# Optimization experiments

Measured on AMD Instinct MI355X. Metric: run time of the kernel, lower is better.

Reference implementation:

```python
import jax, jax.numpy as jnp
import numpy as np

MODEL_DIM = 1024
NUM_HEADS = 16
HEAD_DIM = MODEL_DIM // NUM_HEADS
ROPE_BASE = 10000.0


def apply_rope_full(x):
    # RoPE applied over the FULL model_dim (before head split), interleaved pairs.
    B, S, D = x.shape
    half = D // 2
    inv_freq = 1.0 / (ROPE_BASE ** (jnp.arange(half, dtype=x.dtype) / half))  # [half]
    ang = jnp.arange(S, dtype=x.dtype)[:, None] * inv_freq[None, :]           # [S, half]
    cos, sin = jnp.cos(ang), jnp.sin(ang)
    x1 = x[..., 0::2]  # [B,S,half]
    x2 = x[..., 1::2]
    r1 = x1 * cos - x2 * sin
    r2 = x1 * sin + x2 * cos
    # re-interleave
    return jnp.stack([r1, r2], axis=-1).reshape(B, S, D)


def setup_inputs() -> dict:
    key = jax.random.key(0)
    ks = jax.random.split(key, 9)
    B, S, D = 4, 2048, MODEL_DIM
    sc = 1.0 / np.sqrt(D)
    inp = {
        "X": jax.random.normal(ks[0], (B, S, D), dtype=jnp.float32),
        "Wq": jax.random.normal(ks[1], (D, D), dtype=jnp.float32) * sc,
        "bq": jnp.zeros((D,), dtype=jnp.float32),
        "Wk": jax.random.normal(ks[2], (D, D), dtype=jnp.float32) * sc,
        "bk": jnp.zeros((D,), dtype=jnp.float32),
        "Wv": jax.random.normal(ks[3], (D, D), dtype=jnp.float32) * sc,
        "bv": jnp.zeros((D,), dtype=jnp.float32),
        "Wo": jax.random.normal(ks[4], (D, D), dtype=jnp.float32) * sc,
        "bo": jnp.zeros((D,), dtype=jnp.float32),
    }
    return inp


def reference(X, Wq, bq, Wk, bk, Wv, bv, Wo, bo):
    B, S, D = X.shape
    H, hd = NUM_HEADS, HEAD_DIM
    q = apply_rope_full(X @ Wq + bq)  # [B,S,D], RoPE on full dim as in source
    k = apply_rope_full(X @ Wk + bk)
    v = X @ Wv + bv
    # split heads (contiguous slices d1:d2 == reshape to [B,S,H,hd])
    qh = q.reshape(B, S, H, hd)
    kh = k.reshape(B, S, H, hd)
    vh = v.reshape(B, S, H, hd)
    scale = 1.0 / jnp.sqrt(jnp.asarray(hd, dtype=X.dtype))
    scores = jnp.einsum("bqhd,bkhd->bhqk", qh, kh) * scale  # [B,H,S,S]
    causal = jnp.tril(jnp.ones((S, S), dtype=bool))
    scores = jnp.where(causal[None, None], scores, -jnp.inf)
    weights = jax.nn.softmax(scores, axis=-1)
    attn = jnp.einsum("bhqk,bkhd->bqhd", weights, vh).reshape(B, S, D)
    return attn @ Wo + bo
```

## Files before the change

kernel.cpp:

```cpp
#include <hip/hip_runtime.h>

typedef unsigned short u16;
typedef unsigned int   u32;
typedef __attribute__((ext_vector_type(4))) float f32x4;
typedef __attribute__((ext_vector_type(8))) short short8;

#define MODEL_DIM 1024
#define SEQ 2048
#define BATCH 4
#define NHEAD 16
#define HDIM 64
#define MTOT (BATCH*SEQ)
#define ELEMS ((size_t)MTOT*MODEL_DIM)

__device__ __forceinline__ u16 f2bf(float f) {
    u32 u = __float_as_uint(f);
    u = (u + 0x7fffu + ((u >> 16) & 1u)) >> 16;
    return (u16)u;
}
__device__ __forceinline__ u32 pack2(float a, float b) {
    return (u32)f2bf(a) | ((u32)f2bf(b) << 16);
}
__device__ __forceinline__ u32 cvtpk(float lo, float hi) {
    u32 r;
    asm("v_cvt_pk_bf16_f32 %0, %1, %2" : "=v"(r) : "v"(lo), "v"(hi));
    return r;
}
__device__ __forceinline__ float exp2a(float x) {
    float r;
    asm("v_exp_f32 %0, %1" : "=v"(r) : "v"(x));
    return r;
}

#define GLOAD16(g, l) __builtin_amdgcn_global_load_lds(                        \
        (const __attribute__((address_space(1))) unsigned int*)(g),            \
        (__attribute__((address_space(3))) unsigned int*)(l), 16, 0, 0)

__global__ __launch_bounds__(256) void prep_k(const float* __restrict__ X,
                                              u16* __restrict__ Xb,
                                              const float* __restrict__ Wq,
                                              const float* __restrict__ Wk,
                                              const float* __restrict__ Wv,
                                              const float* __restrict__ Wo,
                                              u16* __restrict__ Wt) {
    const int bid = blockIdx.x, t = threadIdx.x;
    if (bid < 8192) {
        size_t i = ((size_t)bid * 256 + t) * 4;
        float4 v = *(const float4*)(X + i);
        uint2 o; o.x = pack2(v.x, v.y); o.y = pack2(v.z, v.w);
        *(uint2*)(Xb + i) = o;
        return;
    }
    __shared__ float tile[32][33];
    const int bid2 = bid - 8192;
    const int z = bid2 >> 10, rem = bid2 & 1023;
    const int by = rem >> 5, bx = rem & 31;
    const float* W = (z == 0) ? Wq : (z == 1) ? Wk : (z == 2) ? Wv : Wo;
    const int k0 = by * 32, n0 = bx * 32;
    const int x = t & 31, y = t >> 5;
    for (int i = 0; i < 4; ++i)
        tile[y + i * 8][x] = W[(size_t)(k0 + y + i * 8) * MODEL_DIM + n0 + x];
    __syncthreads();
    u16* out = Wt + ((size_t)z << 20);
    for (int i = 0; i < 4; ++i)
        out[(size_t)(n0 + y + i * 8) * MODEL_DIM + k0 + x] = f2bf(tile[x][y + i * 8]);
}

__global__ __launch_bounds__(512) void gemm256qkv_k(
        const u16* __restrict__ A, const u16* __restrict__ Wt,
        u16* __restrict__ Qb, u16* __restrict__ Kb, u32* __restrict__ VT,
        const float* __restrict__ bq, const float* __restrict__ bk,
        const float* __restrict__ bv) {
    __shared__ __align__(16) u16 Ls[49152];
    const int tid  = threadIdx.x;
    const int wv   = tid >> 6, lane = tid & 63;
    const int l15  = lane & 15, quad = lane >> 4;
    const int wr = wv >> 2, wc = wv & 3;
    const int m0 = blockIdx.x * 256;
    const int region = blockIdx.y >> 3;
    const int n0 = (blockIdx.y & 7) * 128;

    const u16* Ag = A + (size_t)m0 * MODEL_DIM;
    const u16* Bg = Wt + ((size_t)region << 20) + (size_t)n0 * MODEL_DIM;

    f32x4 acc[8][2] = {};

#define STAGE_A(kt, d, q) do {                                                 \
    const int kk0_ = (kt) * 64;                                                \
    int L_ = ((q) * 256 + wc * 64 + lane) * 16;                                \
    int P_ = L_ ^ (((L_ >> 7) & 7) << 4);                                      \
    GLOAD16(Ag + (size_t)(wr * 128 + (P_ >> 7)) * MODEL_DIM + kk0_             \
               + ((P_ & 127) >> 1),                                            \
            &Ls[(d) * 24576 + wr * 8192 + (L_ >> 1)]);                         \
} while (0)
#define STAGE_B(kt, d, q) do {                                                 \
    const int kk0_ = (kt) * 64;                                                \
    int L_ = ((q) * 512 + tid) * 16;                                           \
    int P_ = L_ ^ (((L_ >> 7) & 7) << 4);                                      \
    GLOAD16(Bg + (size_t)(P_ >> 7) * MODEL_DIM + kk0_ + ((P_ & 127) >> 1),     \
            &Ls[(d) * 24576 + 16384 + (L_ >> 1)]);                             \
} while (0)

#define LDA8Q(mf, ks) ({                                                       \
    int P_ = ((mf) * 16 + l15) * 128 + ((ks) * 4 + quad) * 16;                 \
    int L_ = P_ ^ (((P_ >> 7) & 7) << 4);                                      \
    *(const short8*)(ab + (L_ >> 1)); })
#define LDB8Q(nf, ks) ({                                                       \
    int P_ = (wc * 32 + (nf) * 16 + l15) * 128 + ((ks) * 4 + quad) * 16;       \
    int L_ = P_ ^ (((P_ >> 7) & 7) << 4);                                      \
    *(const short8*)(bbQ + (L_ >> 1)); })

#define PHASE_MFMA_Q(MH)                                                       \
    __builtin_amdgcn_s_setprio(1);                                             \
    _Pragma("unroll")                                                          \
    for (int j2 = 0; j2 < 4; ++j2)                                             \
        _Pragma("unroll")                                                      \
        for (int nf2 = 0; nf2 < 2; ++nf2)                                      \
            acc[(MH) * 4 + j2][nf2] = __builtin_amdgcn_mfma_f32_16x16x32_bf16( \
                af[j2], bf[nf2], acc[(MH) * 4 + j2][nf2], 0, 0, 0);            \
    __builtin_amdgcn_s_setprio(0);

    STAGE_A(0, 0, 0); STAGE_B(0, 0, 0);
    STAGE_A(0, 0, 1); STAGE_B(0, 0, 1);
    STAGE_A(0, 0, 2); STAGE_A(0, 0, 3);

    for (int t = 0; t < 16; ++t) {
        const int pp2 = t & 1;
        const u16* ab  = &Ls[pp2 * 24576 + wr * 8192];
        const u16* bbQ = &Ls[pp2 * 24576 + 16384];
        const int dn = pp2 ^ 1;
        const bool more = (t + 1) < 16;
        short8 af[4], bf[2];
        if (more) { STAGE_A(t + 1, dn, 0); STAGE_B(t + 1, dn, 0); }
        if (more) asm volatile("s_waitcnt vmcnt(2)" ::: "memory");
        else      asm volatile("s_waitcnt vmcnt(0)" ::: "memory");
        __builtin_amdgcn_s_barrier();
        __builtin_amdgcn_sched_barrier(0);
        #pragma unroll
        for (int nf = 0; nf < 2; ++nf) bf[nf] = LDB8Q(nf, 0);
        #pragma unroll
        for (int j = 0; j < 4; ++j) af[j] = LDA8Q(j, 0);
        PHASE_MFMA_Q(0)
        __builtin_amdgcn_s_barrier();
        #pragma unroll
        for (int j = 0; j < 4; ++j) af[j] = LDA8Q(4 + j, 0);
        if (more) { STAGE_A(t + 1, dn, 1); STAGE_B(t + 1, dn, 1); }
        __builtin_amdgcn_s_barrier();
        __builtin_amdgcn_sched_barrier(0);
        PHASE_MFMA_Q(1)
        __builtin_amdgcn_s_barrier();
        #pragma unroll
        for (int nf = 0; nf < 2; ++nf) bf[nf] = LDB8Q(nf, 1);
        #pragma unroll
        for (int j = 0; j < 4; ++j) af[j] = LDA8Q(j, 1);
        if (more) STAGE_A(t + 1, dn, 2);
        __builtin_amdgcn_s_barrier();
        __builtin_amdgcn_sched_barrier(0);
        PHASE_MFMA_Q(0)
        __builtin_amdgcn_s_barrier();
        #pragma unroll
        for (int j = 0; j < 4; ++j) af[j] = LDA8Q(4 + j, 1);
        if (more) STAGE_A(t + 1, dn, 3);
        __builtin_amdgcn_s_barrier();
        __builtin_amdgcn_sched_barrier(0);
        PHASE_MFMA_Q(1)
        __builtin_amdgcn_s_barrier();
    }

    if (region < 2) {
        const float* bias = region ? bk : bq;
        u16* dst = region ? Kb : Qb;
        const float qsc = region ? 1.0f : 0.125f * 1.44269504f;
        const float cfr = -0.017989922f;
        float invf[2];
        #pragma unroll
        for (int nf = 0; nf < 2; ++nf) {
            int c = n0 + wc * 32 + nf * 16 + l15;
            invf[nf] = __expf((float)(c >> 1) * cfr);
        }
        const float sgn = (l15 & 1) ? 1.0f : -1.0f;
        #pragma unroll
        for (int mf = 0; mf < 8; ++mf)
            #pragma unroll
            for (int r = 0; r < 4; ++r) {
                size_t rowg = (size_t)(m0 + wr * 128 + mf * 16 + quad * 4 + r);
                float fs = (float)(int)(rowg & 2047);
                #pragma unroll
                for (int nf = 0; nf < 2; ++nf) {
                    int c = n0 + wc * 32 + nf * 16 + l15;
                    float v = acc[mf][nf][r] + bias[c];
                    float mate = __shfl_xor(v, 1, 64);
                    float sn, cs;
                    __sincosf(fs * invf[nf], &sn, &cs);
                    float o = (v * cs + sgn * mate * sn) * qsc;
                    dst[rowg * MODEL_DIM + c] = f2bf(o);
                }
            }
    } else {
        const int b_ = m0 >> 11;
        const int s0 = m0 & 2047;
        #pragma unroll
        for (int nf = 0; nf < 2; ++nf) {
            int c = n0 + wc * 32 + nf * 16 + l15;
            float bvc = bv[c];
            u32* vtrow = VT + (size_t)((b_ * NHEAD + (c >> 6)) * HDIM
                                       + (c & 63)) * (SEQ / 2);
            #pragma unroll
            for (int mf = 0; mf < 8; ++mf) {
                int sb2 = s0 + wr * 128 + mf * 16 + quad * 4;
                uint2 w;
                w.x = cvtpk(acc[mf][nf][0] + bvc, acc[mf][nf][1] + bvc);
                w.y = cvtpk(acc[mf][nf][2] + bvc, acc[mf][nf][3] + bvc);
                *(uint2*)(vtrow + (sb2 >> 1)) = w;
            }
        }
    }
#undef STAGE_A
#undef STAGE_B
#undef LDA8Q
#undef LDB8Q
#undef PHASE_MFMA_Q
}

__global__ __launch_bounds__(512) void gemm256o_k(
        const u16* __restrict__ A, const u16* __restrict__ Wt,
        float* __restrict__ outO, const float* __restrict__ bo) {
    __shared__ __align__(16) u16 Ls[49152];
    const int tid  = threadIdx.x;
    const int wv   = tid >> 6, lane = tid & 63;
    const int l15  = lane & 15, quad = lane >> 4;
    const int wr = wv >> 2, wc = wv & 3;
    const int m0 = blockIdx.x * 256;
    const int n0 = blockIdx.y * 128;

    const u16* Ag = A + (size_t)m0 * MODEL_DIM;
    const u16* Bg = Wt + ((size_t)3 << 20) + (size_t)n0 * MODEL_DIM;

    f32x4 acc[8][2] = {};

#define STAGE_A(kt, d, q) do {                                                 \
    const int kk0_ = (kt) * 64;                                                \
    int L_ = ((q) * 256 + wc * 64 + lane) * 16;                                \
    int P_ = L_ ^ (((L_ >> 7) & 7) << 4);                                      \
    GLOAD16(Ag + (size_t)(wr * 128 + (P_ >> 7)) * MODEL_DIM + kk0_             \
               + ((P_ & 127) >> 1),                                            \
            &Ls[(d) * 24576 + wr * 8192 + (L_ >> 1)]);                         \
} while (0)
#define STAGE_B(kt, d, q) do {                                                 \
    const int kk0_ = (kt) * 64;                                                \
    int L_ = ((q) * 512 + tid) * 16;                                           \
    int P_ = L_ ^ (((L_ >> 7) & 7) << 4);                                      \
    GLOAD16(Bg + (size_t)(P_ >> 7) * MODEL_DIM + kk0_ + ((P_ & 127) >> 1),     \
            &Ls[(d) * 24576 + 16384 + (L_ >> 1)]);                             \
} while (0)

#define LDA8O(mf, ks) ({                                                       \
    int P_ = ((mf) * 16 + l15) * 128 + ((ks) * 4 + quad) * 16;                 \
    int L_ = P_ ^ (((P_ >> 7) & 7) << 4);                                      \
    *(const short8*)(ab + (L_ >> 1)); })
#define LDB8O(nf, ks) ({                                                       \
    int P_ = (wc * 32 + (nf) * 16 + l15) * 128 + ((ks) * 4 + quad) * 16;       \
    int L_ = P_ ^ (((P_ >> 7) & 7) << 4);                                      \
    *(const short8*)(bbO + (L_ >> 1)); })

#define PHASE_MFMA_O(MH)                                                       \
    __builtin_amdgcn_s_setprio(1);                                             \
    _Pragma("unroll")                                                          \
    for (int j2 = 0; j2 < 4; ++j2)                                             \
        _Pragma("unroll")                                                      \
        for (int nf2 = 0; nf2 < 2; ++nf2)                                      \
            acc[(MH) * 4 + j2][nf2] = __builtin_amdgcn_mfma_f32_16x16x32_bf16( \
                af[j2], bf[nf2], acc[(MH) * 4 + j2][nf2], 0, 0, 0);            \
    __builtin_amdgcn_s_setprio(0);

    STAGE_A(0, 0, 0); STAGE_B(0, 0, 0);
    STAGE_A(0, 0, 1); STAGE_B(0, 0, 1);
    STAGE_A(0, 0, 2); STAGE_A(0, 0, 3);

    for (int t = 0; t < 16; ++t) {
        const int pp2 = t & 1;
        const u16* ab  = &Ls[pp2 * 24576 + wr * 8192];
        const u16* bbO = &Ls[pp2 * 24576 + 16384];
        const int dn = pp2 ^ 1;
        const bool more = (t + 1) < 16;
        short8 af[4], bf[2];
        if (more) { STAGE_A(t + 1, dn, 0); STAGE_B(t + 1, dn, 0); }
        if (more) asm volatile("s_waitcnt vmcnt(2)" ::: "memory");
        else      asm volatile("s_waitcnt vmcnt(0)" ::: "memory");
        __builtin_amdgcn_s_barrier();
        __builtin_amdgcn_sched_barrier(0);
        #pragma unroll
        for (int nf = 0; nf < 2; ++nf) bf[nf] = LDB8O(nf, 0);
        #pragma unroll
        for (int j = 0; j < 4; ++j) af[j] = LDA8O(j, 0);
        PHASE_MFMA_O(0)
        __builtin_amdgcn_s_barrier();
        #pragma unroll
        for (int j = 0; j < 4; ++j) af[j] = LDA8O(4 + j, 0);
        if (more) { STAGE_A(t + 1, dn, 1); STAGE_B(t + 1, dn, 1); }
        __builtin_amdgcn_s_barrier();
        __builtin_amdgcn_sched_barrier(0);
        PHASE_MFMA_O(1)
        __builtin_amdgcn_s_barrier();
        #pragma unroll
        for (int nf = 0; nf < 2; ++nf) bf[nf] = LDB8O(nf, 1);
        #pragma unroll
        for (int j = 0; j < 4; ++j) af[j] = LDA8O(j, 1);
        if (more) STAGE_A(t + 1, dn, 2);
        __builtin_amdgcn_s_barrier();
        __builtin_amdgcn_sched_barrier(0);
        PHASE_MFMA_O(0)
        __builtin_amdgcn_s_barrier();
        #pragma unroll
        for (int j = 0; j < 4; ++j) af[j] = LDA8O(4 + j, 1);
        if (more) STAGE_A(t + 1, dn, 3);
        __builtin_amdgcn_s_barrier();
        __builtin_amdgcn_sched_barrier(0);
        PHASE_MFMA_O(1)
        __builtin_amdgcn_s_barrier();
    }

    #pragma unroll
    for (int mf = 0; mf < 8; ++mf)
        #pragma unroll
        for (int r = 0; r < 4; ++r) {
            size_t rowg = (size_t)(m0 + wr * 128 + mf * 16 + quad * 4 + r);
            #pragma unroll
            for (int nf = 0; nf < 2; ++nf) {
                int colg = n0 + wc * 32 + nf * 16 + l15;
                outO[rowg * MODEL_DIM + colg] = acc[mf][nf][r] + bo[colg];
            }
        }
#undef STAGE_A
#undef STAGE_B
#undef LDA8O
#undef LDB8O
#undef PHASE_MFMA_O
}

__global__ __launch_bounds__(256, 2) void attn_k(const u16* __restrict__ Qb,
                                                 const u16* __restrict__ Kb,
                                                 const u32* __restrict__ VT32,
                                                 u16* __restrict__ Ob) {
    __shared__ __align__(16) u16 Ks[2][64 * 64];
    __shared__ __align__(16) u16 Vs[2][64 * 64];
    __shared__ __align__(16) u16 Pl[4 * 32 * 72];
    const int tid  = threadIdx.x;
    const int wave = tid >> 6, lane = tid & 63;
    const int l15  = lane & 15, quad = lane >> 4;
    const int j = blockIdx.x;
    const int h = blockIdx.y, b = blockIdx.z;
    u16* pw = &Pl[wave * 32 * 72];

    const int key0 = tid >> 3;
    const int c8   = (tid & 7) * 8;
    const int c4   = (tid & 7) * 4;
    const int lko  = key0 * 64 + (((tid & 7) ^ (key0 & 7)) * 8);
    const u16* kgp = Kb + (size_t)(b * SEQ) * MODEL_DIM + h * HDIM;
    const u32* vgp = VT32 + (size_t)((b * NHEAD + h) * HDIM) * (SEQ / 2);

    int bufc = 0;
    for (int pp = 0; pp < 2; ++pp) {
        const int qt = pp ? j : 15 - j;
        const int q0 = qt * 128;
        const int qbase = q0 + wave * 32;

        short8 qfr[2][2];
        for (int qf = 0; qf < 2; ++qf)
            for (int ks = 0; ks < 2; ++ks)
                qfr[qf][ks] = *(const short8*)(Qb
                    + (size_t)(b * SEQ + qbase + qf * 16 + l15) * MODEL_DIM
                    + h * HDIM + ks * 32 + quad * 8);

        float m_i[2] = {-1e30f, -1e30f}, l_i[2] = {0.f, 0.f};
        f32x4 o_acc[4][2] = {};

        const int nkt = (q0 + 128) >> 6;
        uint4 kr0 = *(const uint4*)(kgp + (size_t)key0 * MODEL_DIM + c8);
        uint4 kr1 = *(const uint4*)(kgp + (size_t)(key0 + 32) * MODEL_DIM + c8);
        uint4 vr0 = *(const uint4*)(vgp + (size_t)key0 * (SEQ / 2) + c4);
        uint4 vr1 = *(const uint4*)(vgp + (size_t)(key0 + 32) * (SEQ / 2) + c4);

        for (int kt = 0; kt < nkt; ++kt) {
            const int k0 = kt * 64;
            u16* ksb = Ks[bufc];
            u16* vsb = Vs[bufc];
            *(uint4*)(&ksb[lko])        = kr0;
            *(uint4*)(&ksb[lko + 2048]) = kr1;
            *(uint4*)(&vsb[lko])        = vr0;
            *(uint4*)(&vsb[lko + 2048]) = vr1;
            __syncthreads();

            if (kt + 1 < nkt) {
                const int kn = k0 + 64;
                kr0 = *(const uint4*)(kgp + (size_t)(kn + key0) * MODEL_DIM + c8);
                kr1 = *(const uint4*)(kgp + (size_t)(kn + key0 + 32) * MODEL_DIM + c8);
                vr0 = *(const uint4*)(vgp + (size_t)key0 * (SEQ / 2) + (kn >> 1) + c4);
                vr1 = *(const uint4*)(vgp + (size_t)(key0 + 32) * (SEQ / 2)
                                      + (kn >> 1) + c4);
            }

            if (k0 <= qbase + 31) {
                f32x4 s[4][2] = {};
                for (int ks = 0; ks < 2; ++ks) {
                    short8 kfr[4];
                    for (int kf = 0; kf < 4; ++kf)
                        kfr[kf] = *(const short8*)(&ksb[(kf * 16 + l15) * 64
                                      + (((ks * 4 + quad) ^ (l15 & 7)) * 8)]);
                    __builtin_amdgcn_s_setprio(1);
                    for (int kf = 0; kf < 4; ++kf)
                        for (int qf = 0; qf < 2; ++qf)
                            s[kf][qf] = __builtin_amdgcn_mfma_f32_16x16x32_bf16(
                                            kfr[kf], qfr[qf][ks], s[kf][qf], 0, 0, 0);
                    __builtin_amdgcn_s_setprio(0);
                }
                for (int qf = 0; qf < 2; ++qf) {
                    int qg = qbase + qf * 16 + l15;
                    if (k0 + 63 > qbase + qf * 16) {
                        for (int kf = 0; kf < 4; ++kf)
                            for (int r = 0; r < 4; ++r)
                                if (k0 + kf * 16 + quad * 4 + r > qg)
                                    s[kf][qf][r] = -1e30f;
                    }
                    float t0 = fmaxf(fmaxf(s[0][qf][0], s[0][qf][1]),
                                     fmaxf(s[0][qf][2], s[0][qf][3]));
                    float t1 = fmaxf(fmaxf(s[1][qf][0], s[1][qf][1]),
                                     fmaxf(s[1][qf][2], s[1][qf][3]));
                    float t2 = fmaxf(fmaxf(s[2][qf][0], s[2][qf][1]),
                                     fmaxf(s[2][qf][2], s[2][qf][3]));
                    float t3 = fmaxf(fmaxf(s[3][qf][0], s[3][qf][1]),
                                     fmaxf(s[3][qf][2], s[3][qf][3]));
                    float rmax = fmaxf(fmaxf(t0, t1), fmaxf(t2, t3));
                    rmax = fmaxf(rmax, __shfl_xor(rmax, 16, 64));
                    rmax = fmaxf(rmax, __shfl_xor(rmax, 32, 64));
                    if (!__all(rmax <= m_i[qf] + 8.0f)) {
                        float mn = fmaxf(m_i[qf], rmax);
                        float alpha = exp2a(m_i[qf] - mn);
                        m_i[qf] = mn;
                        l_i[qf] *= alpha;
                        for (int dt = 0; dt < 4; ++dt)
                            for (int r = 0; r < 4; ++r) o_acc[dt][qf][r] *= alpha;
                    }
                    float mref = m_i[qf];
                    float psum = 0.f;
                    for (int kf = 0; kf < 4; ++kf)
                        for (int r = 0; r < 4; ++r) {
                            float p = exp2a(s[kf][qf][r] - mref);
                            s[kf][qf][r] = p;
                            psum += p;
                        }
                    psum += __shfl_xor(psum, 16, 64);
                    psum += __shfl_xor(psum, 32, 64);
                    l_i[qf] += psum;
                    for (int kf = 0; kf < 4; ++kf) {
                        uint2 w;
                        w.x = cvtpk(s[kf][qf][0], s[kf][qf][1]);
                        w.y = cvtpk(s[kf][qf][2], s[kf][qf][3]);
                        *(uint2*)(&pw[(qf * 16 + l15) * 72 + kf * 16 + quad * 4]) = w;
                    }
                }
                for (int ks = 0; ks < 2; ++ks) {
                    short8 pfr[2], vfr[4];
                    for (int qf = 0; qf < 2; ++qf)
                        pfr[qf] = *(const short8*)(&pw[(qf * 16 + l15) * 72
                                                       + ks * 32 + quad * 8]);
                    for (int dt = 0; dt < 4; ++dt)
                        vfr[dt] = *(const short8*)(&vsb[(dt * 16 + l15) * 64
                                      + (((ks * 4 + quad) ^ (l15 & 7)) * 8)]);
                    __builtin_amdgcn_s_setprio(1);
                    for (int dt = 0; dt < 4; ++dt)
                        for (int qf = 0; qf < 2; ++qf)
                            o_acc[dt][qf] = __builtin_amdgcn_mfma_f32_16x16x32_bf16(
                                                vfr[dt], pfr[qf], o_acc[dt][qf], 0, 0, 0);
                    __builtin_amdgcn_s_setprio(0);
                }
            }
            bufc ^= 1;
        }

        for (int qf = 0; qf < 2; ++qf) {
            float rl = 1.f / l_i[qf];
            int q = qbase + qf * 16 + l15;
            for (int dt = 0; dt < 4; ++dt) {
                uint2 w;
                w.x = cvtpk(o_acc[dt][qf][0] * rl, o_acc[dt][qf][1] * rl);
                w.y = cvtpk(o_acc[dt][qf][2] * rl, o_acc[dt][qf][3] * rl);
                *(uint2*)(&Ob[(size_t)(b * SEQ + q) * MODEL_DIM
                              + h * HDIM + dt * 16 + quad * 4]) = w;
            }
        }
    }
}

extern "C" void kernel_launch(void* const* d_in, const int* in_sizes, int n_in,
                              void* d_out, int out_size, void* d_ws, size_t ws_size,
                              hipStream_t stream) {
    const float* X  = (const float*)d_in[0];
    const float* Wq = (const float*)d_in[1];
    const float* bq = (const float*)d_in[2];
    const float* Wk = (const float*)d_in[3];
    const float* bk = (const float*)d_in[4];
    const float* Wv = (const float*)d_in[5];
    const float* bv = (const float*)d_in[6];
    const float* Wo = (const float*)d_in[7];
    const float* bo = (const float*)d_in[8];
    float* out = (float*)d_out;

    char* ws = (char*)d_ws;
    u16* Xb   = (u16*)ws;
    u16* Ob   = (u16*)ws;
    u16* Wt   = (u16*)(ws + 16777216);
    u16* Qb   = (u16*)(ws + 25165824);
    u16* Kb   = (u16*)(ws + 41943040);
    u32* VT32 = (u32*)(ws + 75497472);

    prep_k<<<dim3(12288), dim3(256), 0, stream>>>(X, Xb, Wq, Wk, Wv, Wo, Wt);
    gemm256qkv_k<<<dim3(32, 24), dim3(512), 0, stream>>>(Xb, Wt, Qb, Kb, VT32,
                                                         bq, bk, bv);
    attn_k<<<dim3(8, 16, 4), dim3(256), 0, stream>>>(Qb, Kb, VT32, Ob);
    gemm256o_k<<<dim3(32, 8), dim3(512), 0, stream>>>(Ob, Wt, out, bo);
}
```

Before: 256.2 us.

## Split attention query tile across eight waves of sixteen rows each

The attention kernel now launches 512 threads per block, and each of eight waves handles 16 query rows instead of four waves handling 32. Each thread loads one K and one V vector per tile instead of two, and the per-wave P staging buffer shrinks to match. This is meant to raise wave-level parallelism and cut per-wave register pressure and causal-mask waste. In exchange, each wave gets half the K/V fragment reuse from LDS per MFMA and must coordinate more waves at each barrier.

```diff
diff --git a/kernel.cpp b/kernel.cpp
--- a/kernel.cpp
+++ b/kernel.cpp
@@ -338,19 +338,19 @@
 #undef PHASE_MFMA_O
 }
 
-__global__ __launch_bounds__(256, 2) void attn_k(const u16* __restrict__ Qb,
+__global__ __launch_bounds__(512, 2) void attn_k(const u16* __restrict__ Qb,
                                                  const u16* __restrict__ Kb,
                                                  const u32* __restrict__ VT32,
                                                  u16* __restrict__ Ob) {
     __shared__ __align__(16) u16 Ks[2][64 * 64];
     __shared__ __align__(16) u16 Vs[2][64 * 64];
-    __shared__ __align__(16) u16 Pl[4 * 32 * 72];
+    __shared__ __align__(16) u16 Pl[8 * 16 * 72];
     const int tid  = threadIdx.x;
     const int wave = tid >> 6, lane = tid & 63;
     const int l15  = lane & 15, quad = lane >> 4;
     const int j = blockIdx.x;
     const int h = blockIdx.y, b = blockIdx.z;
-    u16* pw = &Pl[wave * 32 * 72];
+    u16* pw = &Pl[wave * 16 * 72];
 
     const int key0 = tid >> 3;
     const int c8   = (tid & 7) * 8;
@@ -363,45 +363,37 @@
     for (int pp = 0; pp < 2; ++pp) {
         const int qt = pp ? j : 15 - j;
         const int q0 = qt * 128;
-        const int qbase = q0 + wave * 32;
-
-        short8 qfr[2][2];
-        for (int qf = 0; qf < 2; ++qf)
-            for (int ks = 0; ks < 2; ++ks)
-                qfr[qf][ks] = *(const short8*)(Qb
-                    + (size_t)(b * SEQ + qbase + qf * 16 + l15) * MODEL_DIM
-                    + h * HDIM + ks * 32 + quad * 8);
-
-        float m_i[2] = {-1e30f, -1e30f}, l_i[2] = {0.f, 0.f};
-        f32x4 o_acc[4][2] = {};
+        const int qbase = q0 + wave * 16;
+
+        short8 qfr[2];
+        for (int ks = 0; ks < 2; ++ks)
+            qfr[ks] = *(const short8*)(Qb
+                + (size_t)(b * SEQ + qbase + l15) * MODEL_DIM
+                + h * HDIM + ks * 32 + quad * 8);
+
+        float m_i = -1e30f, l_i = 0.f;
+        f32x4 o_acc[4] = {};
 
         const int nkt = (q0 + 128) >> 6;
         uint4 kr0 = *(const uint4*)(kgp + (size_t)key0 * MODEL_DIM + c8);
-        uint4 kr1 = *(const uint4*)(kgp + (size_t)(key0 + 32) * MODEL_DIM + c8);
         uint4 vr0 = *(const uint4*)(vgp + (size_t)key0 * (SEQ / 2) + c4);
-        uint4 vr1 = *(const uint4*)(vgp + (size_t)(key0 + 32) * (SEQ / 2) + c4);
 
         for (int kt = 0; kt < nkt; ++kt) {
             const int k0 = kt * 64;
             u16* ksb = Ks[bufc];
             u16* vsb = Vs[bufc];
-            *(uint4*)(&ksb[lko])        = kr0;
-            *(uint4*)(&ksb[lko + 2048]) = kr1;
-            *(uint4*)(&vsb[lko])        = vr0;
-            *(uint4*)(&vsb[lko + 2048]) = vr1;
+            *(uint4*)(&ksb[lko]) = kr0;
+            *(uint4*)(&vsb[lko]) = vr0;
             __syncthreads();
 
             if (kt + 1 < nkt) {
                 const int kn = k0 + 64;
                 kr0 = *(const uint4*)(kgp + (size_t)(kn + key0) * MODEL_DIM + c8);
-                kr1 = *(const uint4*)(kgp + (size_t)(kn + key0 + 32) * MODEL_DIM + c8);
                 vr0 = *(const uint4*)(vgp + (size_t)key0 * (SEQ / 2) + (kn >> 1) + c4);
-                vr1 = *(const uint4*)(vgp + (size_t)(key0 + 32) * (SEQ / 2)
-                                      + (kn >> 1) + c4);
             }
 
-            if (k0 <= qbase + 31) {
-                f32x4 s[4][2] = {};
+            if (k0 <= qbase + 15) {
+                f32x4 s[4] = {};
                 for (int ks = 0; ks < 2; ++ks) {
                     short8 kfr[4];
                     for (int kf = 0; kf < 4; ++kf)
@@ -409,82 +401,71 @@
                                       + (((ks * 4 + quad) ^ (l15 & 7)) * 8)]);
                     __builtin_amdgcn_s_setprio(1);
                     for (int kf = 0; kf < 4; ++kf)
-                        for (int qf = 0; qf < 2; ++qf)
-                            s[kf][qf] = __builtin_amdgcn_mfma_f32_16x16x32_bf16(
-                                            kfr[kf], qfr[qf][ks], s[kf][qf], 0, 0, 0);
+                        s[kf] = __builtin_amdgcn_mfma_f32_16x16x32_bf16(
+                                    kfr[kf], qfr[ks], s[kf], 0, 0, 0);
                     __builtin_amdgcn_s_setprio(0);
                 }
-                for (int qf = 0; qf < 2; ++qf) {
-                    int qg = qbase + qf * 16 + l15;
-                    if (k0 + 63 > qbase + qf * 16) {
-                        for (int kf = 0; kf < 4; ++kf)
-                            for (int r = 0; r < 4; ++r)
-                                if (k0 + kf * 16 + quad * 4 + r > qg)
-                                    s[kf][qf][r] = -1e30f;
+                const int qg = qbase + l15;
+                if (k0 + 63 > qbase) {
+                    for (int kf = 0; kf < 4; ++kf)
+                        for (int r = 0; r < 4; ++r)
+                            if (k0 + kf * 16 + quad * 4 + r > qg)
+                                s[kf][r] = -1e30f;
+                }
+                float t0 = fmaxf(fmaxf(s[0][0], s[0][1]), fmaxf(s[0][2], s[0][3]));
+                float t1 = fmaxf(fmaxf(s[1][0], s[1][1]), fmaxf(s[1][2], s[1][3]));
+                float t2 = fmaxf(fmaxf(s[2][0], s[2][1]), fmaxf(s[2][2], s[2][3]));
+                float t3 = fmaxf(fmaxf(s[3][0], s[3][1]), fmaxf(s[3][2], s[3][3]));
+                float rmax = fmaxf(fmaxf(t0, t1), fmaxf(t2, t3));
+                rmax = fmaxf(rmax, __shfl_xor(rmax, 16, 64));
+                rmax = fmaxf(rmax, __shfl_xor(rmax, 32, 64));
+                if (!__all(rmax <= m_i + 8.0f)) {
+                    float mn = fmaxf(m_i, rmax);
+                    float alpha = exp2a(m_i - mn);
+                    m_i = mn;
+                    l_i *= alpha;
+                    for (int dt = 0; dt < 4; ++dt)
+                        for (int r = 0; r < 4; ++r) o_acc[dt][r] *= alpha;
+                }
+                float psum = 0.f;
+                for (int kf = 0; kf < 4; ++kf)
+                    for (int r = 0; r < 4; ++r) {
+                        float p = exp2a(s[kf][r] - m_i);
+                        s[kf][r] = p;
+                        psum += p;
                     }
-                    float t0 = fmaxf(fmaxf(s[0][qf][0], s[0][qf][1]),
-                                     fmaxf(s[0][qf][2], s[0][qf][3]));
-                    float t1 = fmaxf(fmaxf(s[1][qf][0], s[1][qf][1]),
-                                     fmaxf(s[1][qf][2], s[1][qf][3]));
-                    float t2 = fmaxf(fmaxf(s[2][qf][0], s[2][qf][1]),
-                                     fmaxf(s[2][qf][2], s[2][qf][3]));
-                    float t3 = fmaxf(fmaxf(s[3][qf][0], s[3][qf][1]),
-                                     fmaxf(s[3][qf][2], s[3][qf][3]));
-                    float rmax = fmaxf(fmaxf(t0, t1), fmaxf(t2, t3));
-                    rmax = fmaxf(rmax, __shfl_xor(rmax, 16, 64));
-                    rmax = fmaxf(rmax, __shfl_xor(rmax, 32, 64));
-                    if (!__all(rmax <= m_i[qf] + 8.0f)) {
-                        float mn = fmaxf(m_i[qf], rmax);
-                        float alpha = exp2a(m_i[qf] - mn);
-                        m_i[qf] = mn;
-                        l_i[qf] *= alpha;
-                        for (int dt = 0; dt < 4; ++dt)
-                            for (int r = 0; r < 4; ++r) o_acc[dt][qf][r] *= alpha;
-                    }
-                    float mref = m_i[qf];
-                    float psum = 0.f;
-                    for (int kf = 0; kf < 4; ++kf)
-                        for (int r = 0; r < 4; ++r) {
-                            float p = exp2a(s[kf][qf][r] - mref);
-                            s[kf][qf][r] = p;
-                            psum += p;
-                        }
-                    psum += __shfl_xor(psum, 16, 64);
-                    psum += __shfl_xor(psum, 32, 64);
-                    l_i[qf] += psum;
-                    for (int kf = 0; kf < 4; ++kf) {
-                        uint2 w;
-                        w.x = cvtpk(s[kf][qf][0], s[kf][qf][1]);
-                        w.y = cvtpk(s[kf][qf][2], s[kf][qf][3]);
-                        *(uint2*)(&pw[(qf * 16 + l15) * 72 + kf * 16 + quad * 4]) = w;
-                    }
+                psum += __shfl_xor(psum, 16, 64);
+                psum += __shfl_xor(psum, 32, 64);
+                l_i += psum;
+                for (int kf = 0; kf < 4; ++kf) {
+                    uint2 w;
+                    w.x = cvtpk(s[kf][0], s[kf][1]);
+                    w.y = cvtpk(s[kf][2], s[kf][3]);
+                    *(uint2*)(&pw[l15 * 72 + kf * 16 + quad * 4]) = w;
                 }
                 for (int ks = 0; ks < 2; ++ks) {
-                    short8 pfr[2], vfr[4];
-                    for (int qf = 0; qf < 2; ++qf)
-                        pfr[qf] = *(const short8*)(&pw[(qf * 16 + l15) * 72
-                                                       + ks * 32 + quad * 8]);
+                    short8 pfr, vfr[4];
+                    pfr = *(const short8*)(&pw[l15 * 72 + ks * 32 + quad * 8]);
                     for (int dt = 0; dt < 4; ++dt)
                         vfr[dt] = *(const short8*)(&vsb[(dt * 16 + l15) * 64
                                       + (((ks * 4 + quad) ^ (l15 & 7)) * 8)]);
                     __builtin_amdgcn_s_setprio(1);
                     for (int dt = 0; dt < 4; ++dt)
-                        for (int qf = 0; qf < 2; ++qf)
-                            o_acc[dt][qf] = __builtin_amdgcn_mfma_f32_16x16x32_bf16(
-                                                vfr[dt], pfr[qf], o_acc[dt][qf], 0, 0, 0);
+                        o_acc[dt] = __builtin_amdgcn_mfma_f32_16x16x32_bf16(
+                                        vfr[dt], pfr, o_acc[dt], 0, 0, 0);
                     __builtin_amdgcn_s_setprio(0);
                 }
             }
             bufc ^= 1;
         }
 
-        for (int qf = 0; qf < 2; ++qf) {
-            float rl = 1.f / l_i[qf];
-            int q = qbase + qf * 16 + l15;
+        {
+            float rl = 1.f / l_i;
+            int q = qbase + l15;
             for (int dt = 0; dt < 4; ++dt) {
                 uint2 w;
-                w.x = cvtpk(o_acc[dt][qf][0] * rl, o_acc[dt][qf][1] * rl);
-                w.y = cvtpk(o_acc[dt][qf][2] * rl, o_acc[dt][qf][3] * rl);
+                w.x = cvtpk(o_acc[dt][0] * rl, o_acc[dt][1] * rl);
+                w.y = cvtpk(o_acc[dt][2] * rl, o_acc[dt][3] * rl);
                 *(uint2*)(&Ob[(size_t)(b * SEQ + q) * MODEL_DIM
                               + h * HDIM + dt * 16 + quad * 4]) = w;
             }
@@ -517,6 +498,6 @@
     prep_k<<<dim3(12288), dim3(256), 0, stream>>>(X, Xb, Wq, Wk, Wv, Wo, Wt);
     gemm256qkv_k<<<dim3(32, 24), dim3(512), 0, stream>>>(Xb, Wt, Qb, Kb, VT32,
                                                          bq, bk, bv);
-    attn_k<<<dim3(8, 16, 4), dim3(256), 0, stream>>>(Qb, Kb, VT32, Ob);
+    attn_k<<<dim3(8, 16, 4), dim3(512), 0, stream>>>(Qb, Kb, VT32, Ob);
     gemm256o_k<<<dim3(32, 8), dim3(512), 0, stream>>>(Ob, Wt, out, bo);
 }
```

Result: no change. 255.2 us (-0.4%).
